# Kernel tuning notes

Measured on AMD Instinct MI355X. Metric: run time of the kernel, lower is better.

## Reference

```python
import jax, jax.numpy as jnp
import numpy as np

BETA = 0.25


def setup_inputs() -> dict:
    key = jax.random.key(0)
    k1, k2, k3, k4 = jax.random.split(key, 4)
    B, D, T, H, W = 2, 256, 8, 32, 32
    K = 8192
    z = jax.random.normal(k1, (B, D, T, H, W), dtype=jnp.float32)
    # nn.init.normal_(embedding.weight, mean=0, std=emb_dim ** -0.5)
    emb_w = jax.random.normal(k2, (K, D), dtype=jnp.float32) * (D ** -0.5)
    # torch Linear default init ~ U(-1/sqrt(in), 1/sqrt(in)); scaled normal is fine for a reference
    w1 = jax.random.normal(k3, (D, D), dtype=jnp.float32) * (D ** -0.5)
    w2 = jax.random.normal(k4, (D, D), dtype=jnp.float32) * (D ** -0.5)
    return {"z": z, "emb_w": emb_w, "w1": w1, "w2": w2}


def reference(z, emb_w, w1, w2):
    B, D, T, H, W = z.shape
    K = emb_w.shape[0]
    # permute to channels-last and flatten: [B,T,H,W,D] -> [N,D]
    z_cl = jnp.transpose(z, (0, 2, 3, 4, 1))
    z_flat = z_cl.reshape(-1, D)
    N = z_flat.shape[0]
    # simvq: Linear -> GELU (exact) -> Linear, both bias-free
    quant_codebook = jax.nn.gelu(emb_w @ w1.T, approximate=False) @ w2.T  # [K, D]
    # pairwise squared L2 distances [N, K]
    d = (
        jnp.sum(z_flat ** 2, axis=1, keepdims=True)
        + jnp.sum(quant_codebook ** 2, axis=1)
        - 2.0 * (z_flat @ quant_codebook.T)
    )
    mean_distance = jnp.mean(d)
    idx = jnp.argmin(d, axis=1)  # [N]
    # gather == one-hot @ codebook
    z_q_flat = quant_codebook[idx]  # [N, D]
    z_q = z_q_flat.reshape(z_cl.shape)
    # VQ loss with stop-gradients
    loss = jnp.mean((jax.lax.stop_gradient(z_q) - z_cl) ** 2) + BETA * jnp.mean(
        (z_q - jax.lax.stop_gradient(z_cl)) ** 2
    )
    # straight-through estimator
    z_q = z_cl + jax.lax.stop_gradient(z_q - z_cl)
    # perplexity from code usage histogram (== mean of one-hot encodings)
    counts = jnp.zeros((K,), dtype=jnp.float32).at[idx].add(1.0)
    e_mean = counts / N
    perplexity = jnp.exp(-jnp.sum(e_mean * jnp.log(e_mean + 1e-10)))
    # back to channels-first [B, D, T, H, W]
    z_q = jnp.transpose(z_q, (0, 4, 1, 2, 3))
    return z_q, loss, perplexity, mean_distance
```

## Files before the change

kernel.cpp:

```cpp
#include <hip/hip_runtime.h>
#include <math.h>

#define BATCH 2
#define DIM   256
#define THW   8192
#define NTOK  16384
#define KCB   8192
#define OUTQ  4194304
#define CAP   2000000
#define SCAP  5600

typedef short short8 __attribute__((ext_vector_type(8)));
typedef float f32x4 __attribute__((ext_vector_type(4)));

__device__ __forceinline__ unsigned short f2bf_rn(float v) {
    unsigned u = __float_as_uint(v);
    unsigned r = u + 0x7FFFu + ((u >> 16) & 1u);
    return (unsigned short)(r >> 16);
}
__device__ __forceinline__ float bf2f(unsigned short b) {
    return __uint_as_float((unsigned)b << 16);
}
__device__ __forceinline__ void gl2lds16(const unsigned short* g, unsigned short* l) {
    __builtin_amdgcn_global_load_lds(
        (const __attribute__((address_space(1))) void*)g,
        (__attribute__((address_space(3))) void*)l, 16, 0, 0);
}

__global__ void k_splitW(const float* __restrict__ w1, const float* __restrict__ w2,
                         unsigned short* __restrict__ W1s, unsigned short* __restrict__ W2s,
                         int* __restrict__ counts,
                         unsigned* __restrict__ tileMaxC, unsigned* __restrict__ tileMaxCl,
                         float* __restrict__ accums,
                         float* __restrict__ partialZ, float* __restrict__ partialC) {
    int bid = blockIdx.x;
    int t = threadIdx.x;
    if (bid < 32) {
        counts[bid * 256 + t] = 0;
    } else if (bid == 32) {
        if (t < 64) { tileMaxC[t] = 0u; tileMaxCl[t] = 0u; }
        if (t >= 64 && t < 72) accums[t - 64] = 0.f;
    } else if (bid == 33) {
        partialZ[t] = 0.f;
    } else if (bid == 34) {
        partialC[t] = 0.f;
    }
    int row = bid & 255;
    const float* src = (bid >> 8) ? w2 : w1;
    unsigned short* dst = ((bid >> 8) ? W2s : W1s) + (size_t)row * 768;
    float v = src[row * 256 + t];
    unsigned short hb = f2bf_rn(v);
    unsigned short lb = f2bf_rn(v - bf2f(hb));
    dst[t] = hb;
    dst[256 + t] = hb;
    dst[512 + t] = lb;
}

__global__ void k_buildA(const float* __restrict__ z,
                         unsigned short* __restrict__ Ahi,
                         unsigned short* __restrict__ Alo,
                         float* __restrict__ zsq,
                         float* __restrict__ sA, float* __restrict__ sB,
                         float* __restrict__ partialZ,
                         unsigned long long* __restrict__ packed,
                         unsigned long long* __restrict__ packed2) {
    __shared__ ushort2 tile[64][65];
    __shared__ float zacc[64];
    __shared__ float lacc[64];
    __shared__ float pz[256];
    int t = threadIdx.x;
    int n0 = blockIdx.x * 64;
    int b = n0 >> 13;
    int thw0 = n0 & 8191;
    if (t < 64) {
        zacc[t] = 0.f; lacc[t] = 0.f;
        packed[n0 + t] = ~0ull;
        packed2[n0 + t] = ~0ull;
    }
    pz[t] = 0.f;
    __syncthreads();
    int nn_r = t & 63, dg = t >> 6;
    float a1 = 0.f, a2 = 0.f;
    for (int dc = 0; dc < 256; dc += 64) {
        for (int r = 0; r < 16; ++r) {
            int dd = r * 4 + dg;
            float v = z[((size_t)(b * 256 + dc + dd)) * 8192 + thw0 + nn_r];
            unsigned short hb = f2bf_rn(v);
            float hf = bf2f(hb);
            unsigned short lb = f2bf_rn(v - hf);
            float lf = bf2f(lb);
            tile[dd][nn_r] = make_ushort2(hb, lb);
            a1 += v * v;
            a2 += lf * lf;
        }
        __syncthreads();
        int kk = t & 63, ng = t >> 6;
        float dimsum = 0.f;
        for (int i2 = 0; i2 < 16; ++i2) {
            int nn = ng + i2 * 4;
            ushort2 hl = tile[kk][nn];
            size_t base = (size_t)(n0 + nn) * 256;
            Ahi[base + dc + kk] = hl.x;
            Alo[base + dc + kk] = hl.y;
            dimsum += bf2f(hl.x) + bf2f(hl.y);
        }
        atomicAdd(&pz[dc + kk], dimsum);
        __syncthreads();
    }
    atomicAdd(&zacc[nn_r], a1);
    atomicAdd(&lacc[nn_r], a2);
    __syncthreads();
    if (t < 64) {
        zsq[n0 + t] = zacc[t];
        sA[n0 + t] = 2.1f * sqrtf(lacc[t]);
        sB[n0 + t] = 2.1f * sqrtf(zacc[t]);
    }
    atomicAdd(&partialZ[t], pz[t]);
}

__global__ void k_buildE(const float* __restrict__ emb, unsigned short* __restrict__ E) {
    int t = threadIdx.x;
    int row = blockIdx.x * 4 + (t >> 6);
    int e4 = (t & 63) * 4;
    float4 v = *(const float4*)&emb[(size_t)row * 256 + e4];
    ushort4 hi, lo;
    hi.x = f2bf_rn(v.x); lo.x = f2bf_rn(v.x - bf2f(hi.x));
    hi.y = f2bf_rn(v.y); lo.y = f2bf_rn(v.y - bf2f(hi.y));
    hi.z = f2bf_rn(v.z); lo.z = f2bf_rn(v.z - bf2f(hi.z));
    hi.w = f2bf_rn(v.w); lo.w = f2bf_rn(v.w - bf2f(hi.w));
    size_t base = (size_t)row * 768;
    *(ushort4*)&E[base + e4] = hi;
    *(ushort4*)&E[base + 256 + e4] = lo;
    *(ushort4*)&E[base + 512 + e4] = hi;
}

template <int GELU>
__global__ __launch_bounds__(256) void k_mlp(const unsigned short* __restrict__ A,
                                             const unsigned short* __restrict__ B,
                                             unsigned short* __restrict__ Hs,
                                             float* __restrict__ C_t) {
    __shared__ __align__(16) char smem[32768];
    unsigned short* Asm = (unsigned short*)smem;
    unsigned short* Bsm = (unsigned short*)(smem + 16384);

    int t = threadIdx.x;
    int lane = t & 63;
    int w = t >> 6;
    int wm = w >> 1, wn = w & 1;
    int m0 = blockIdx.y * 128;
    int n0 = blockIdx.x * 128;

    int rA = w * 8 + (lane >> 3);
    int ch_l = lane & 7;
    int ch_g = ch_l ^ (lane >> 3);
    const unsigned short* gA = A + (size_t)(m0 + rA) * 768 + ch_g * 8;
    const unsigned short* gB = B + (size_t)(n0 + rA) * 768 + ch_g * 8;
    unsigned short* lA = &Asm[rA * 64 + ch_l * 8];
    unsigned short* lB = &Bsm[rA * 64 + ch_l * 8];

    f32x4 acc[4][4];
#pragma unroll
    for (int i = 0; i < 4; ++i)
#pragma unroll
        for (int j = 0; j < 4; ++j)
            acc[i][j] = f32x4{0.f, 0.f, 0.f, 0.f};

#pragma unroll
    for (int i = 0; i < 4; ++i) {
        gl2lds16(gA + (size_t)(32 * i) * 768, lA + 32 * i * 64);
        gl2lds16(gB + (size_t)(32 * i) * 768, lB + 32 * i * 64);
    }
    __syncthreads();

    int l15 = lane & 15;
    int quad = lane >> 4;
    int sw = l15 & 7;
    for (int kc = 0; kc < 12; ++kc) {
#pragma unroll
        for (int kk = 0; kk < 2; ++kk) {
            short8 a[4], b[4];
#pragma unroll
            for (int i = 0; i < 4; ++i)
                a[i] = *(const short8*)&Asm[(wm * 64 + i * 16 + l15) * 64 +
                                            (((kk * 4 + quad) ^ sw) * 8)];
#pragma unroll
            for (int j = 0; j < 4; ++j)
                b[j] = *(const short8*)&Bsm[(wn * 64 + j * 16 + l15) * 64 +
                                            (((kk * 4 + quad) ^ sw) * 8)];
#pragma unroll
            for (int i = 0; i < 4; ++i)
#pragma unroll
                for (int j = 0; j < 4; ++j)
                    acc[i][j] = __builtin_amdgcn_mfma_f32_16x16x32_bf16(a[i], b[j], acc[i][j], 0, 0, 0);
        }
        __syncthreads();
        if (kc < 11) {
            int ko = (kc + 1) * 64;
#pragma unroll
            for (int i = 0; i < 4; ++i) {
                gl2lds16(gA + (size_t)(32 * i) * 768 + ko, lA + 32 * i * 64);
                gl2lds16(gB + (size_t)(32 * i) * 768 + ko, lB + 32 * i * 64);
            }
            __syncthreads();
        }
    }

#pragma unroll
    for (int i = 0; i < 4; ++i) {
#pragma unroll
        for (int reg = 0; reg < 4; ++reg) {
            int mrow = m0 + wm * 64 + i * 16 + quad * 4 + reg;
#pragma unroll
            for (int j = 0; j < 4; ++j) {
                int ncol = n0 + wn * 64 + j * 16 + l15;
                float h = acc[i][j][reg];
                if (GELU) {
                    float g = 0.5f * h * (1.f + erff(h * 0.70710678118654752f));
                    unsigned short hb = f2bf_rn(g);
                    unsigned short lb = f2bf_rn(g - bf2f(hb));
                    size_t base = (size_t)mrow * 768;
                    Hs[base + ncol] = hb;
                    Hs[base + 256 + ncol] = lb;
                    Hs[base + 512 + ncol] = hb;
                } else {
                    C_t[(size_t)mrow * 8192 + ncol] = h;
                }
            }
        }
    }
}

__global__ void k_buildB(const float* __restrict__ C_t,
                         unsigned short* __restrict__ Bhi,
                         unsigned short* __restrict__ Blo,
                         float* __restrict__ csq,
                         float* __restrict__ sC, float* __restrict__ sCl,
                         unsigned* __restrict__ tileMaxC, unsigned* __restrict__ tileMaxCl,
                         float* __restrict__ accums, float* __restrict__ partialC) {
    __shared__ ushort2 tile[64][65];
    __shared__ float kacc[64];
    __shared__ float lacc[64];
    __shared__ float pc[256];
    int t = threadIdx.x;
    int k0 = blockIdx.x * 64;
    if (t < 64) { kacc[t] = 0.f; lacc[t] = 0.f; }
    pc[t] = 0.f;
    __syncthreads();
    int nn_r = t & 63, dg = t >> 6;
    float a1 = 0.f, a2 = 0.f;
    for (int dc = 0; dc < 256; dc += 64) {
        for (int r = 0; r < 16; ++r) {
            int dd = r * 4 + dg;
            float v = C_t[(size_t)(dc + dd) * KCB + k0 + nn_r];
            unsigned short hb = f2bf_rn(v);
            float hf = bf2f(hb);
            unsigned short lb = f2bf_rn(v - hf);
            float lf = bf2f(lb);
            tile[dd][nn_r] = make_ushort2(hb, lb);
            a1 += v * v;
            a2 += lf * lf;
        }
        __syncthreads();
        int kk = t & 63, ng = t >> 6;
        float dimsum = 0.f;
        for (int i2 = 0; i2 < 16; ++i2) {
            int nn = ng + i2 * 4;
            ushort2 hl = tile[kk][nn];
            size_t base = (size_t)(k0 + nn) * 256;
            Bhi[base + dc + kk] = hl.x;
            Blo[base + dc + kk] = hl.y;
            dimsum += bf2f(hl.x) + bf2f(hl.y);
        }
        atomicAdd(&pc[dc + kk], dimsum);
        __syncthreads();
    }
    atomicAdd(&kacc[nn_r], a1);
    atomicAdd(&lacc[nn_r], a2);
    __syncthreads();
    if (t < 64) {
        float c2 = kacc[t], l2 = lacc[t];
        float sc = sqrtf(c2), sl = sqrtf(l2);
        csq[k0 + t] = c2;
        sC[k0 + t] = sc;
        sCl[k0 + t] = sl;
        int tl = blockIdx.x >> 1;
        atomicMax(&tileMaxC[tl], __float_as_uint(sc));
        atomicMax(&tileMaxCl[tl], __float_as_uint(sl));
        atomicMax((unsigned*)&accums[3], __float_as_uint(c2));
        atomicMax((unsigned*)&accums[4], __float_as_uint(l2));
    }
    atomicAdd(&partialC[t], pc[t]);
}

__global__ __launch_bounds__(512, 2) void k_dist_hi(const unsigned short* __restrict__ A,
                                                    const unsigned short* __restrict__ B,
                                                    const float* __restrict__ zsq,
                                                    const float* __restrict__ csq,
                                                    const float* __restrict__ sA,
                                                    const float* __restrict__ sB,
                                                    const unsigned* __restrict__ tileMaxC,
                                                    const unsigned* __restrict__ tileMaxCl,
                                                    unsigned long long* __restrict__ packed,
                                                    float* __restrict__ accums,
                                                    unsigned long long* __restrict__ cand) {
    __shared__ __align__(16) char smem[131072];
    float* sbd     = (float*)smem;
    float* gprev_s = (float*)(smem + 2048);
    float* thr     = (float*)(smem + 3072);
    unsigned* scnt  = (unsigned*)(smem + 4096);
    unsigned* sbase = (unsigned*)(smem + 4100);
    unsigned long long* scand = (unsigned long long*)(smem + 4112);

    int t = threadIdx.x;
    int lane = t & 63;
    int w = t >> 6;
    int wm = w >> 1, wn = w & 1;
    int m0 = blockIdx.x * 256;
    int n0 = blockIdx.y * 256;

    int rA0 = w * 8 + (lane >> 3);
    int ch_l = lane & 7;
    int ch_g = ch_l ^ (lane >> 3);
    const unsigned short* gA = A + (size_t)(m0 + rA0) * 256 + ch_g * 8;
    const unsigned short* gB = B + (size_t)(n0 + rA0) * 256 + ch_g * 8;
    unsigned short* smemU = (unsigned short*)smem;
    unsigned short* lA = smemU + rA0 * 64 + ch_l * 8;
    unsigned short* lB = smemU + 16384 + rA0 * 64 + ch_l * 8;

    int l15 = lane & 15;
    int quad = lane >> 4;
    int sw = l15 & 7;

    float M1 = sqrtf(accums[3]);
    float M2 = sqrtf(accums[4]);
    float msC  = fmaxf(__uint_as_float(tileMaxC[2 * blockIdx.y]),
                       __uint_as_float(tileMaxC[2 * blockIdx.y + 1]));
    float msCl = fmaxf(__uint_as_float(tileMaxCl[2 * blockIdx.y]),
                       __uint_as_float(tileMaxCl[2 * blockIdx.y + 1]));
    float cv[8];
    int cols[8];
#pragma unroll
    for (int j = 0; j < 8; ++j) {
        int cloc = wn * 128 + j * 16 + l15;
        cols[j] = n0 + cloc;
        cv[j] = csq[cols[j]];
    }

    f32x4 acc[4][8];
#pragma unroll
    for (int i = 0; i < 4; ++i)
#pragma unroll
        for (int j = 0; j < 8; ++j)
            acc[i][j] = f32x4{0.f, 0.f, 0.f, 0.f};

#define STAGE(B_, KO)                                                       \
    {                                                                       \
        int off_ = (B_) * 32768;                                            \
        _Pragma("unroll")                                                   \
        for (int i_ = 0; i_ < 4; ++i_)                                      \
            gl2lds16(gA + (size_t)(64 * i_) * 256 + (KO),                   \
                     lA + off_ + 64 * i_ * 64);                             \
        _Pragma("unroll")                                                   \
        for (int i_ = 0; i_ < 4; ++i_)                                      \
            gl2lds16(gB + (size_t)(64 * i_) * 256 + (KO),                   \
                     lB + off_ + 64 * i_ * 64);                             \
    }

    STAGE(0, 0)
    __syncthreads();

    int cur = 0;
    for (int kc = 0; kc < 4; ++kc) {
        if (kc < 3) STAGE(cur ^ 1, (kc + 1) * 64)
        const unsigned short* Ar = smemU + cur * 32768;
        const unsigned short* Br = Ar + 16384;
#pragma unroll
        for (int kk = 0; kk < 2; ++kk) {
            short8 a[4], b[8];
#pragma unroll
            for (int i = 0; i < 4; ++i)
                a[i] = *(const short8*)&Ar[(wm * 64 + i * 16 + l15) * 64 +
                                            (((kk * 4 + quad) ^ sw) * 8)];
#pragma unroll
            for (int j = 0; j < 8; ++j)
                b[j] = *(const short8*)&Br[(wn * 128 + j * 16 + l15) * 64 +
                                            (((kk * 4 + quad) ^ sw) * 8)];
#pragma unroll
            for (int i = 0; i < 4; ++i)
#pragma unroll
                for (int j = 0; j < 8; ++j)
                    acc[i][j] = __builtin_amdgcn_mfma_f32_16x16x32_bf16(a[i], b[j], acc[i][j], 0, 0, 0);
        }
        __syncthreads();
        cur ^= 1;
    }
#undef STAGE

    if (t == 0) *scnt = 0;
    if (t < 256) {
        const unsigned* hp = (const unsigned*)&packed[m0 + t];
        gprev_s[t] = __uint_as_float(__atomic_load_n(hp + 1, __ATOMIC_RELAXED));
    }
#pragma unroll
    for (int i = 0; i < 4; ++i) {
#pragma unroll
        for (int reg = 0; reg < 4; ++reg) {
            int rloc = wm * 64 + i * 16 + quad * 4 + reg;
            float zs = zsq[m0 + rloc];
            float bd = 3.4e38f;
#pragma unroll
            for (int j = 0; j < 8; ++j) {
                float d = (zs + cv[j]) - 2.0f * acc[i][j][reg];
                acc[i][j][reg] = d;
                bd = fminf(bd, d);
            }
#pragma unroll
            for (int off = 1; off < 16; off <<= 1)
                bd = fminf(bd, __shfl_xor(bd, off, 64));
            if (l15 == 0) sbd[wn * 256 + rloc] = bd;
        }
    }
    __syncthreads();
    if (t < 256) {
        float bd = fminf(sbd[t], sbd[256 + t]);
        atomicMin(&packed[m0 + t], (unsigned long long)__float_as_uint(bd) << 32);
        float g = fminf(bd, gprev_s[t]);
        thr[t] = g + 1e-3f + sA[m0 + t] * (M1 + msC) + sB[m0 + t] * (M2 + msCl);
    }
    __syncthreads();
    unsigned* cnt = (unsigned*)&accums[2];
#pragma unroll
    for (int i = 0; i < 4; ++i) {
#pragma unroll
        for (int reg = 0; reg < 4; ++reg) {
            int rloc = wm * 64 + i * 16 + quad * 4 + reg;
            float tr = thr[rloc];
            bool p[8];
            bool any = false;
#pragma unroll
            for (int j = 0; j < 8; ++j) {
                p[j] = acc[i][j][reg] <= tr;
                any |= p[j];
            }
            if (__ballot(any)) {
                unsigned rbits = (unsigned)((m0 + rloc) << 13);
#pragma unroll
                for (int j = 0; j < 8; ++j) {
                    if (p[j]) {
                        unsigned long long entry =
                            ((unsigned long long)__float_as_uint(acc[i][j][reg]) << 32) |
                            (rbits | (unsigned)cols[j]);
                        unsigned pos = atomicAdd(scnt, 1u);
                        if (pos < SCAP) scand[pos] = entry;
                        else {
                            unsigned gp2 = atomicAdd(cnt, 1u);
                            if (gp2 < CAP) cand[gp2] = entry;
                        }
                    }
                }
            }
        }
    }
    __syncthreads();
    if (t == 0) {
        unsigned m = *scnt;
        if (m > SCAP) m = SCAP;
        *scnt = m;
        *sbase = atomicAdd(cnt, m);
    }
    __syncthreads();
    {
        unsigned m = *scnt, b0 = *sbase;
        for (unsigned u = t; u < m; u += 512)
            if (b0 + u < CAP) cand[b0 + u] = scand[u];
    }
}

__global__ __launch_bounds__(256) void k_rescore(const unsigned long long* __restrict__ cand,
                                                 const unsigned short* __restrict__ Ahi,
                                                 const unsigned short* __restrict__ Alo,
                                                 const unsigned short* __restrict__ Bhi,
                                                 const unsigned short* __restrict__ Blo,
                                                 const float* __restrict__ zsq,
                                                 const float* __restrict__ csq,
                                                 const float* __restrict__ sA,
                                                 const float* __restrict__ sB,
                                                 const float* __restrict__ sC,
                                                 const float* __restrict__ sCl,
                                                 const unsigned long long* __restrict__ packed,
                                                 unsigned long long* __restrict__ packed2,
                                                 const float* __restrict__ accums) {
    unsigned total = *(const unsigned*)&accums[2];
    if (total > CAP) total = CAP;
    float M1 = sqrtf(accums[3]);
    float M2 = sqrtf(accums[4]);
    int lane = threadIdx.x & 63;
    unsigned wv = blockIdx.x * 4 + (threadIdx.x >> 6);
    unsigned nw = gridDim.x * 4;
    for (unsigned e = wv; e < total; e += nw) {
        unsigned long long ent = cand[e];
        float dhi = __uint_as_float((unsigned)(ent >> 32));
        unsigned nk = (unsigned)ent;
        int n = (nk >> 13) & 16383;
        int k = nk & 8191;
        float g = __uint_as_float((unsigned)(packed[n] >> 32));
        float marg = g + 1e-3f + sA[n] * (M1 + sC[k]) + sB[n] * (M2 + sCl[k]);
        if (dhi > marg) continue;
        ushort4 zh = *((const ushort4*)(Ahi + (size_t)n * 256) + lane);
        ushort4 zl = *((const ushort4*)(Alo + (size_t)n * 256) + lane);
        ushort4 ch = *((const ushort4*)(Bhi + (size_t)k * 256) + lane);
        ushort4 cl = *((const ushort4*)(Blo + (size_t)k * 256) + lane);
        float s = (bf2f(zh.x) + bf2f(zl.x)) * (bf2f(ch.x) + bf2f(cl.x))
                + (bf2f(zh.y) + bf2f(zl.y)) * (bf2f(ch.y) + bf2f(cl.y))
                + (bf2f(zh.z) + bf2f(zl.z)) * (bf2f(ch.z) + bf2f(cl.z))
                + (bf2f(zh.w) + bf2f(zl.w)) * (bf2f(ch.w) + bf2f(cl.w));
#pragma unroll
        for (int off = 1; off < 64; off <<= 1)
            s += __shfl_xor(s, off, 64);
        if (lane == 0) {
            float dd = (zsq[n] + csq[k]) - 2.0f * s;
            unsigned long long p =
                ((unsigned long long)__float_as_uint(dd) << 32) | (unsigned)k;
            atomicMin(&packed2[n], p);
        }
    }
}

__global__ void k_zqloss(const float* __restrict__ z, const float* __restrict__ C_t,
                         const unsigned long long* __restrict__ packed2,
                         float* __restrict__ out, float* __restrict__ loss_sum,
                         int* __restrict__ counts) {
    __shared__ float red[256];
    int bid = blockIdx.x;
    int b = bid >> 8;
    int d = bid & 255;
    int t = threadIdx.x;
    const float* crow = C_t + (size_t)d * KCB;
    const unsigned long long* pb = packed2 + (size_t)b * THW;
    size_t base = ((size_t)(b * DIM + d)) * THW;
    float lsum = 0.f;
    for (int it = 0; it < 8; ++it) {
        int thw = it * 1024 + t * 4;
        ulonglong2 p01 = *(const ulonglong2*)&pb[thw];
        ulonglong2 p23 = *(const ulonglong2*)&pb[thw + 2];
        int i0 = (int)(unsigned)p01.x & 8191;
        int i1 = (int)(unsigned)p01.y & 8191;
        int i2 = (int)(unsigned)p23.x & 8191;
        int i3 = (int)(unsigned)p23.y & 8191;
        float4 zz = *(const float4*)&z[base + thw];
        float4 v;
        v.x = crow[i0]; v.y = crow[i1]; v.z = crow[i2]; v.w = crow[i3];
        *(float4*)&out[base + thw] = v;
        float d0 = v.x - zz.x, d1 = v.y - zz.y, d2 = v.z - zz.z, d3 = v.w - zz.w;
        lsum += d0 * d0 + d1 * d1 + d2 * d2 + d3 * d3;
        if (d == 0) {
            atomicAdd(&counts[i0], 1);
            atomicAdd(&counts[i1], 1);
            atomicAdd(&counts[i2], 1);
            atomicAdd(&counts[i3], 1);
        }
    }
    red[t] = lsum;
    __syncthreads();
    for (int s = 128; s > 0; s >>= 1) {
        if (t < s) red[t] += red[t + s];
        __syncthreads();
    }
    if (t == 0) atomicAdd(loss_sum, red[0]);
}

__global__ void k_scalars(const int* __restrict__ counts,
                          const float* __restrict__ accums,
                          const float* __restrict__ zsq, const float* __restrict__ csq,
                          const float* __restrict__ partialZ,
                          const float* __restrict__ partialC,
                          float* __restrict__ out_tail) {
    __shared__ double redd[256];
    __shared__ float redf[256];
    int t = threadIdx.x;
    double szsq = 0.0, scsq = 0.0;
    for (int n = t; n < NTOK; n += 256) szsq += (double)zsq[n];
    for (int k = t; k < KCB; k += 256) scsq += (double)csq[k];
    float SZ = partialZ[t];
    float SC = partialC[t];
    double total = 8192.0 * szsq + 16384.0 * scsq - 2.0 * (double)SZ * (double)SC;
    redd[t] = total;
    float s = 0.f;
    for (int k = t; k < KCB; k += 256) {
        float e = (float)counts[k] * (1.0f / 16384.0f);
        s += e * logf(e + 1e-10f);
    }
    redf[t] = s;
    __syncthreads();
    for (int st = 128; st > 0; st >>= 1) {
        if (t < st) { redd[t] += redd[t + st]; redf[t] += redf[t + st]; }
        __syncthreads();
    }
    if (t == 0) {
        out_tail[0] = 1.25f * accums[1] / 4194304.0f;
        out_tail[1] = expf(-redf[0]);
        out_tail[2] = (float)(redd[0] / (16384.0 * 8192.0));
    }
}

extern "C" void kernel_launch(void* const* d_in, const int* in_sizes, int n_in,
                              void* d_out, int out_size, void* d_ws, size_t ws_size,
                              hipStream_t stream) {
    const float* z     = (const float*)d_in[0];
    const float* emb_w = (const float*)d_in[1];
    const float* w1    = (const float*)d_in[2];
    const float* w2    = (const float*)d_in[3];
    float* out = (float*)d_out;

    char* w = (char*)d_ws;
    unsigned short* Ahi = (unsigned short*)(w + 0);
    unsigned short* Alo = (unsigned short*)(w + 8388608);
    unsigned short* Ebf = (unsigned short*)(w + 16777216);
    unsigned short* Bhi = (unsigned short*)(w + 29360128);
    unsigned short* Blo = (unsigned short*)(w + 33554432);
    unsigned short* W1s = (unsigned short*)(w + 37748736);
    unsigned short* W2s = (unsigned short*)(w + 38141952);
    float* zsq   = (float*)(w + 38535168);
    float* sA    = (float*)(w + 38666240);
    float* sB    = (float*)(w + 38731776);
    float* csq   = (float*)(w + 38797312);
    float* sC    = (float*)(w + 38862848);
    float* sCl   = (float*)(w + 38895616);
    unsigned long long* packed  = (unsigned long long*)(w + 38928384);
    unsigned long long* packed2 = (unsigned long long*)(w + 39059456);
    int*   counts = (int*)(w + 39256064);
    float* partialZ = (float*)(w + 39288832);
    float* partialC = (float*)(w + 39550976);
    unsigned* tileMaxC  = (unsigned*)(w + 39682048);
    unsigned* tileMaxCl = (unsigned*)(w + 39682304);
    float* accums = (float*)(w + 39682560);

    float* C_t = (float*)Ebf;
    unsigned short* Hs = (unsigned short*)d_out;
    unsigned long long* cand = (unsigned long long*)d_out;

    k_splitW<<<512, 256, 0, stream>>>(w1, w2, W1s, W2s, counts,
                                      tileMaxC, tileMaxCl, accums, partialZ, partialC);
    k_buildA<<<NTOK / 64, 256, 0, stream>>>(z, Ahi, Alo, zsq, sA, sB, partialZ,
                                            packed, packed2);
    k_buildE<<<KCB / 4, 256, 0, stream>>>(emb_w, Ebf);

    k_mlp<1><<<dim3(2, KCB / 128), 256, 0, stream>>>(Ebf, W1s, Hs, nullptr);
    k_mlp<0><<<dim3(KCB / 128, 2), 256, 0, stream>>>(W2s, Hs, nullptr, C_t);

    k_buildB<<<KCB / 64, 256, 0, stream>>>(C_t, Bhi, Blo, csq, sC, sCl,
                                           tileMaxC, tileMaxCl, accums, partialC);

    k_dist_hi<<<dim3(NTOK / 256, KCB / 256), 512, 0, stream>>>(
        Ahi, Bhi, zsq, csq, sA, sB, tileMaxC, tileMaxCl, packed, accums, cand);

    k_rescore<<<1024, 256, 0, stream>>>(cand, Ahi, Alo, Bhi, Blo, zsq, csq,
                                        sA, sB, sC, sCl, packed, packed2, accums);

    k_zqloss<<<BATCH * DIM, 256, 0, stream>>>(z, C_t, packed2, out, accums + 1, counts);
    k_scalars<<<1, 256, 0, stream>>>(counts, accums, zsq, csq, partialZ, partialC, out + OUTQ);
}
```

Measured before the change: 411.4 us.

## Compact passing rescore candidates per block and spread histogram atomics across blocks

The rescore kernel now lets each thread test one candidate against its margin and compacts the survivors into a shared-memory queue with ballot and popcount. Waves then run the 64-lane dot product only on queued survivors, so whole waves no longer load and test one candidate at a time and mostly skip. Candidates are split into contiguous chunks per block, which adds block barriers per chunk of 256. The code-usage histogram atomics move from the d==0 blocks, which each did 16K atomics serially, to 32 atomics in every block.

New measurement: 380.3 us. 1.08x faster.

```diff
diff --git a/kernel.cpp b/kernel.cpp
--- a/kernel.cpp
+++ b/kernel.cpp
@@ -490,39 +490,73 @@
                                                  const unsigned long long* __restrict__ packed,
                                                  unsigned long long* __restrict__ packed2,
                                                  const float* __restrict__ accums) {
+    __shared__ unsigned long long q[256];
+    __shared__ unsigned qn;
     unsigned total = *(const unsigned*)&accums[2];
     if (total > CAP) total = CAP;
     float M1 = sqrtf(accums[3]);
     float M2 = sqrtf(accums[4]);
-    int lane = threadIdx.x & 63;
-    unsigned wv = blockIdx.x * 4 + (threadIdx.x >> 6);
-    unsigned nw = gridDim.x * 4;
-    for (unsigned e = wv; e < total; e += nw) {
-        unsigned long long ent = cand[e];
-        float dhi = __uint_as_float((unsigned)(ent >> 32));
-        unsigned nk = (unsigned)ent;
-        int n = (nk >> 13) & 16383;
-        int k = nk & 8191;
-        float g = __uint_as_float((unsigned)(packed[n] >> 32));
-        float marg = g + 1e-3f + sA[n] * (M1 + sC[k]) + sB[n] * (M2 + sCl[k]);
-        if (dhi > marg) continue;
-        ushort4 zh = *((const ushort4*)(Ahi + (size_t)n * 256) + lane);
-        ushort4 zl = *((const ushort4*)(Alo + (size_t)n * 256) + lane);
-        ushort4 ch = *((const ushort4*)(Bhi + (size_t)k * 256) + lane);
-        ushort4 cl = *((const ushort4*)(Blo + (size_t)k * 256) + lane);
-        float s = (bf2f(zh.x) + bf2f(zl.x)) * (bf2f(ch.x) + bf2f(cl.x))
-                + (bf2f(zh.y) + bf2f(zl.y)) * (bf2f(ch.y) + bf2f(cl.y))
-                + (bf2f(zh.z) + bf2f(zl.z)) * (bf2f(ch.z) + bf2f(cl.z))
-                + (bf2f(zh.w) + bf2f(zl.w)) * (bf2f(ch.w) + bf2f(cl.w));
-#pragma unroll
-        for (int off = 1; off < 64; off <<= 1)
-            s += __shfl_xor(s, off, 64);
-        if (lane == 0) {
-            float dd = (zsq[n] + csq[k]) - 2.0f * s;
-            unsigned long long p =
-                ((unsigned long long)__float_as_uint(dd) << 32) | (unsigned)k;
-            atomicMin(&packed2[n], p);
-        }
+    int t = threadIdx.x;
+    int lane = t & 63;
+    int w = t >> 6;
+    unsigned per = (total + gridDim.x - 1) / gridDim.x;
+    unsigned e0 = blockIdx.x * per;
+    unsigned e1 = e0 + per;
+    if (e1 > total) e1 = total;
+    for (unsigned base = e0; base < e1; base += 256) {
+        if (t == 0) qn = 0;
+        __syncthreads();
+        unsigned e = base + (unsigned)t;
+        bool pass = false;
+        unsigned long long ent = 0;
+        if (e < e1) {
+            ent = cand[e];
+            float dhi = __uint_as_float((unsigned)(ent >> 32));
+            unsigned nk = (unsigned)ent;
+            int n = (nk >> 13) & 16383;
+            int k = nk & 8191;
+            float g = __uint_as_float((unsigned)(packed[n] >> 32));
+            float marg = g + 1e-3f + sA[n] * (M1 + sC[k]) + sB[n] * (M2 + sCl[k]);
+            pass = (dhi <= marg);
+        }
+        unsigned long long mask = __ballot(pass);
+        if (mask) {
+            unsigned cw = (unsigned)__popcll(mask);
+            unsigned wbase = 0;
+            if (lane == 0) wbase = atomicAdd(&qn, cw);
+            wbase = __shfl(wbase, 0, 64);
+            if (pass) {
+                unsigned pos = wbase +
+                    (unsigned)__popcll(mask & ((1ull << lane) - 1ull));
+                q[pos] = ent;
+            }
+        }
+        __syncthreads();
+        unsigned m = qn;
+        for (unsigned i = (unsigned)w; i < m; i += 4) {
+            unsigned long long e2 = q[i];
+            unsigned nk = (unsigned)e2;
+            int n = (nk >> 13) & 16383;
+            int k = nk & 8191;
+            ushort4 zh = *((const ushort4*)(Ahi + (size_t)n * 256) + lane);
+            ushort4 zl = *((const ushort4*)(Alo + (size_t)n * 256) + lane);
+            ushort4 ch = *((const ushort4*)(Bhi + (size_t)k * 256) + lane);
+            ushort4 cl = *((const ushort4*)(Blo + (size_t)k * 256) + lane);
+            float s = (bf2f(zh.x) + bf2f(zl.x)) * (bf2f(ch.x) + bf2f(cl.x))
+                    + (bf2f(zh.y) + bf2f(zl.y)) * (bf2f(ch.y) + bf2f(cl.y))
+                    + (bf2f(zh.z) + bf2f(zl.z)) * (bf2f(ch.z) + bf2f(cl.z))
+                    + (bf2f(zh.w) + bf2f(zl.w)) * (bf2f(ch.w) + bf2f(cl.w));
+#pragma unroll
+            for (int off = 1; off < 64; off <<= 1)
+                s += __shfl_xor(s, off, 64);
+            if (lane == 0) {
+                float dd = (zsq[n] + csq[k]) - 2.0f * s;
+                unsigned long long p =
+                    ((unsigned long long)__float_as_uint(dd) << 32) | (unsigned)k;
+                atomicMin(&packed2[n], p);
+            }
+        }
+        __syncthreads();
     }
 }
 
@@ -535,6 +569,10 @@
     int b = bid >> 8;
     int d = bid & 255;
     int t = threadIdx.x;
+    if (t < 32) {
+        int kk = (int)(unsigned)packed2[bid * 32 + t] & 8191;
+        atomicAdd(&counts[kk], 1);
+    }
     const float* crow = C_t + (size_t)d * KCB;
     const unsigned long long* pb = packed2 + (size_t)b * THW;
     size_t base = ((size_t)(b * DIM + d)) * THW;
@@ -553,12 +591,6 @@
         *(float4*)&out[base + thw] = v;
         float d0 = v.x - zz.x, d1 = v.y - zz.y, d2 = v.z - zz.z, d3 = v.w - zz.w;
         lsum += d0 * d0 + d1 * d1 + d2 * d2 + d3 * d3;
-        if (d == 0) {
-            atomicAdd(&counts[i0], 1);
-            atomicAdd(&counts[i1], 1);
-            atomicAdd(&counts[i2], 1);
-            atomicAdd(&counts[i3], 1);
-        }
     }
     red[t] = lsum;
     __syncthreads();
```
